# Performance work log

Measured on AMD Instinct MI355X. Metric: run time of the kernel, lower is better.

Reference implementation:

```python
import jax, jax.numpy as jnp
import numpy as np

EMBED_DIM = 1024
NUM_HEADS = 16
DEPTH = 12
HEAD_DIM = EMBED_DIM // NUM_HEADS // 2  # 32
LAMBDA_INIT = float(0.8 - 0.6 * np.exp(-0.3 * DEPTH))
B, T = 2, 2048


def setup_inputs() -> dict:
    key = jax.random.key(0)
    ks = jax.random.split(key, 10)
    s = 0.02
    return {
        "query": jax.random.normal(ks[0], (B, T, EMBED_DIM), jnp.float32),
        "Wq": jax.random.normal(ks[1], (EMBED_DIM, EMBED_DIM), jnp.float32) * s,
        "Wk": jax.random.normal(ks[2], (EMBED_DIM, EMBED_DIM), jnp.float32) * s,
        "Wv": jax.random.normal(ks[3], (EMBED_DIM, EMBED_DIM), jnp.float32) * s,
        "Wo": jax.random.normal(ks[4], (EMBED_DIM, EMBED_DIM), jnp.float32) * s,
        "lambda_q1": jax.random.normal(ks[5], (HEAD_DIM,), jnp.float32) * 0.1,
        "lambda_k1": jax.random.normal(ks[6], (HEAD_DIM,), jnp.float32) * 0.1,
        "lambda_q2": jax.random.normal(ks[7], (HEAD_DIM,), jnp.float32) * 0.1,
        "lambda_k2": jax.random.normal(ks[8], (HEAD_DIM,), jnp.float32) * 0.1,
        "subln_w": jnp.ones((2 * HEAD_DIM,), jnp.float32),
    }


def reference(query, Wq, Wk, Wv, Wo, lambda_q1, lambda_k1, lambda_q2, lambda_k2, subln_w):
    Bsz, Tt, E = query.shape
    H, hd = NUM_HEADS, HEAD_DIM
    scaling = hd ** -0.5
    # projections (torch Linear: x @ W.T), W stored [out, in]
    q = jnp.einsum('bte,fe->btf', query, Wq).reshape(Bsz, Tt, 2 * H, hd).transpose(0, 2, 1, 3)
    k = jnp.einsum('bse,fe->bsf', query, Wk).reshape(Bsz, Tt, 2 * H, hd).transpose(0, 2, 1, 3)
    v = jnp.einsum('bse,fe->bsf', query, Wv).reshape(Bsz, Tt, H, 2 * hd).transpose(0, 2, 1, 3)
    q = q * scaling
    # dual attention map [B, 2H, T, T], softmax in fp32
    scores = jnp.einsum('bhtd,bhsd->bhts', q, k)
    attn_w = jax.nn.softmax(scores.astype(jnp.float32), axis=-1).astype(q.dtype)
    # learned lambda
    lam1 = jnp.exp(jnp.sum(lambda_q1 * lambda_k1))
    lam2 = jnp.exp(jnp.sum(lambda_q2 * lambda_k2))
    lam = lam1 - lam2 + LAMBDA_INIT
    aw = attn_w.reshape(Bsz, H, 2, Tt, Tt)
    aw = aw[:, :, 0] - lam * aw[:, :, 1]  # [B, H, T, T]
    attn = jnp.einsum('bhts,bhsd->bhtd', aw, v)  # [B, H, T, 2*hd]
    # RMSNorm over last dim (fp32), eps=1e-5, elementwise affine
    x32 = attn.astype(jnp.float32)
    normed = (x32 * jax.lax.rsqrt(jnp.mean(x32 * x32, axis=-1, keepdims=True) + 1e-5)).astype(attn.dtype)
    attn = normed * subln_w
    attn = attn * (1.0 - LAMBDA_INIT)
    out = attn.transpose(0, 2, 1, 3).reshape(Bsz, Tt, H * 2 * hd)
    return jnp.einsum('bte,fe->btf', out, Wo)
```

## Files before the change

### kernel.cpp

```cpp
#include <hip/hip_runtime.h>

typedef short bf16x8 __attribute__((ext_vector_type(8)));
typedef float f32x4 __attribute__((ext_vector_type(4)));
typedef float f32x16 __attribute__((ext_vector_type(16)));
typedef unsigned short ushort_t;
typedef unsigned int uint32;

#define LAMBDA_INIT 0.7836057665316245f
#define TT 2048
#define EE 1024

__device__ __forceinline__ ushort_t f2bf(float x) {
  uint32 b = __float_as_uint(x);
  b += 0x7fffu + ((b >> 16) & 1u);
  return (ushort_t)(b >> 16);
}

__device__ __forceinline__ uint32 cvtpk(float lo, float hi) {
  uint32 r;
  asm("v_cvt_pk_bf16_f32 %0, %1, %2" : "=v"(r) : "v"(lo), "v"(hi));
  return r;
}

__device__ __forceinline__ float fexp2(float x) {
#if __has_builtin(__builtin_amdgcn_exp2f)
  return __builtin_amdgcn_exp2f(x);
#else
  return exp2f(x);
#endif
}

__device__ __forceinline__ bf16x8 mkfrag(uint32 a, uint32 b, uint32 c, uint32 d) {
  union { uint32 w[4]; bf16x8 v; } u;
  u.w[0] = a; u.w[1] = b; u.w[2] = c; u.w[3] = d;
  return u.v;
}

__device__ __forceinline__ void gload16(const void* g, void* l) {
  __builtin_amdgcn_global_load_lds(
      (const __attribute__((address_space(1))) uint32*)g,
      (__attribute__((address_space(3))) uint32*)l, 16, 0, 0);
}

__global__ __launch_bounds__(256) void cvt_all(const float* __restrict__ X,
                                               const float* __restrict__ Wq,
                                               const float* __restrict__ Wk,
                                               const float* __restrict__ Wv,
                                               const float* __restrict__ Wo,
                                               ushort_t* __restrict__ out) {
  const int i = blockIdx.x * 256 + threadIdx.x;
  const float* src;
  int off;
  if (i < 1048576)      { src = X;  off = 0; }
  else if (i < 1310720) { src = Wq; off = 1048576; }
  else if (i < 1572864) { src = Wk; off = 1310720; }
  else if (i < 1835008) { src = Wv; off = 1572864; }
  else                  { src = Wo; off = 1835008; }
  const float4 v = reinterpret_cast<const float4*>(src)[i - off];
  ushort4 o;
  o.x = f2bf(v.x); o.y = f2bf(v.y); o.z = f2bf(v.z); o.w = f2bf(v.w);
  reinterpret_cast<ushort4*>(out)[i] = o;
}

template <int MODE>
__global__ __launch_bounds__(256) void gemm_bt(const ushort_t* __restrict__ A,
                                               const ushort_t* __restrict__ B,
                                               void* __restrict__ C,
                                               int M, int N, int K, float scale) {
  __shared__ ushort_t As[128 * 32];
  __shared__ ushort_t Bs[128 * 32];
  const int tid = threadIdx.x;
  const int lane = tid & 63, wid = tid >> 6;
  const int wr = wid >> 1, wc = wid & 1;
  const int r16 = lane & 15, g = lane >> 4;
  const int m0 = blockIdx.x * 128, n0 = blockIdx.y * 128;
  f32x4 acc[4][4] = {};
  for (int k0 = 0; k0 < K; k0 += 32) {
#pragma unroll
    for (int c = 0; c < 2; ++c) {
      int eo = wid * 1024 + c * 512 + lane * 8;
      int row = eo >> 5, col = eo & 31;
      gload16(A + (size_t)(m0 + row) * K + k0 + col, As + wid * 1024 + c * 512);
      gload16(B + (size_t)(n0 + row) * K + k0 + col, Bs + wid * 1024 + c * 512);
    }
    __syncthreads();
    bf16x8 af[4], bfg[4];
#pragma unroll
    for (int m = 0; m < 4; ++m)
      af[m] = *reinterpret_cast<const bf16x8*>(As + (wr * 64 + m * 16 + r16) * 32 + g * 8);
#pragma unroll
    for (int n = 0; n < 4; ++n)
      bfg[n] = *reinterpret_cast<const bf16x8*>(Bs + (wc * 64 + n * 16 + r16) * 32 + g * 8);
#pragma unroll
    for (int m = 0; m < 4; ++m)
#pragma unroll
      for (int n = 0; n < 4; ++n)
        acc[m][n] = __builtin_amdgcn_mfma_f32_16x16x32_bf16(af[m], bfg[n], acc[m][n], 0, 0, 0);
    __syncthreads();
  }
#pragma unroll
  for (int m = 0; m < 4; ++m)
#pragma unroll
    for (int n = 0; n < 4; ++n) {
      if constexpr (MODE == 3) {
        const size_t MN = (size_t)4096 * EE;
        const int col = n0 + wc * 64 + n * 16 + r16;
        const int seg = col >> 10;
        const int cl = col & 1023;
        if (seg == 2) {
          int row0 = m0 + wr * 64 + m * 16 + g * 4;
          int bb = row0 >> 11, t0v = row0 & (TT - 1);
          ushort4 pk;
          pk.x = f2bf(acc[m][n][0]); pk.y = f2bf(acc[m][n][1]);
          pk.z = f2bf(acc[m][n][2]); pk.w = f2bf(acc[m][n][3]);
          *reinterpret_cast<ushort4*>(
              (ushort_t*)C + 2 * MN +
              ((size_t)(bb * 16 + (cl >> 6)) * 64 + (cl & 63)) * TT + t0v) = pk;
        } else {
          const float sc = (seg == 0) ? scale : 1.0f;
          const size_t base = (size_t)seg * MN;
#pragma unroll
          for (int r = 0; r < 4; ++r) {
            int row = m0 + wr * 64 + m * 16 + g * 4 + r;
            ((ushort_t*)C)[base + (size_t)row * EE + cl] = f2bf(acc[m][n][r] * sc);
          }
        }
      } else {
#pragma unroll
        for (int r = 0; r < 4; ++r) {
          int row = m0 + wr * 64 + m * 16 + g * 4 + r;
          int col = n0 + wc * 64 + n * 16 + r16;
          reinterpret_cast<float*>(C)[(size_t)row * N + col] = acc[m][n][r] * scale;
        }
      }
    }
}


#define PHALF(sv, lacc, oT0, oT1, vf)                                                   \
  do {                                                                                  \
    float p_[16];                                                                       \
    _Pragma("unroll") for (int i_ = 0; i_ < 16; ++i_) p_[i_] = fexp2(sv[i_]);           \
    lacc += (((p_[0] + p_[1]) + (p_[2] + p_[3])) + ((p_[4] + p_[5]) + (p_[6] + p_[7]))) \
          + (((p_[8] + p_[9]) + (p_[10] + p_[11])) +                                    \
             ((p_[12] + p_[13]) + (p_[14] + p_[15])));                                  \
    auto wA_ = __builtin_amdgcn_permlane32_swap((int)cvtpk(p_[0], p_[1]),               \
                                                (int)cvtpk(p_[4], p_[5]), false, false);\
    auto wB_ = __builtin_amdgcn_permlane32_swap((int)cvtpk(p_[2], p_[3]),               \
                                                (int)cvtpk(p_[6], p_[7]), false, false);\
    auto wC_ = __builtin_amdgcn_permlane32_swap((int)cvtpk(p_[8], p_[9]),               \
                                                (int)cvtpk(p_[12], p_[13]), false, false);\
    auto wD_ = __builtin_amdgcn_permlane32_swap((int)cvtpk(p_[10], p_[11]),             \
                                                (int)cvtpk(p_[14], p_[15]), false, false);\
    bf16x8 pa0_ = mkfrag(wA_[0], wB_[0], wA_[1], wB_[1]);                               \
    bf16x8 pa1_ = mkfrag(wC_[0], wD_[0], wC_[1], wD_[1]);                               \
    oT0 = __builtin_amdgcn_mfma_f32_32x32x16_bf16(pa0_, vf[0][0], oT0, 0, 0, 0);        \
    oT0 = __builtin_amdgcn_mfma_f32_32x32x16_bf16(pa1_, vf[1][0], oT0, 0, 0, 0);        \
    oT1 = __builtin_amdgcn_mfma_f32_32x32x16_bf16(pa0_, vf[0][1], oT1, 0, 0, 0);        \
    oT1 = __builtin_amdgcn_mfma_f32_32x32x16_bf16(pa1_, vf[1][1], oT1, 0, 0, 0);        \
  } while (0)

#define STAGE(bi, kv0)                                                                  \
  do {                                                                                  \
    const int r8_ = lane >> 3;                                                          \
    const int g_ = (lane & 7) ^ r8_;                                                    \
    _Pragma("unroll") for (int c2_ = 0; c2_ < 2; ++c2_) {                               \
      const int c_ = wid * 2 + c2_;                                                     \
      gload16(Kg + (size_t)((kv0) + c_ * 8 + r8_) * EE + g_ * 8,                        \
              Ksm[bi] + c_ * 512);                                                      \
      gload16(Vg + (size_t)(c_ * 8 + r8_) * TT + (kv0) + g_ * 8,                        \
              Vsm[bi] + c_ * 512);                                                      \
    }                                                                                   \
  } while (0)

__global__ __launch_bounds__(256, 2) void attn_fused(
    const ushort_t* __restrict__ Q, const ushort_t* __restrict__ K,
    const ushort_t* __restrict__ Vt,
    const float* __restrict__ lq1, const float* __restrict__ lk1,
    const float* __restrict__ lq2, const float* __restrict__ lk2,
    const float* __restrict__ w, ushort_t* __restrict__ X2) {
  __shared__ ushort_t Ksm[2][64 * 64];
  __shared__ ushort_t Vsm[2][64 * 64];
  const int tid = threadIdx.x, lane = tid & 63, wid = tid >> 6;
  const int l31 = lane & 31, hh = lane >> 5;
  const int bid = blockIdx.x;
  const int slice = (bid & 7) + 8 * (bid >> 7);
  const int qb = (bid >> 3) & 15;
  const int bb = slice >> 4, h = slice & 15;
  const int q0 = qb * 128 + wid * 32;

  float prod = (lane < 32) ? lq1[l31] * lk1[l31] : lq2[l31] * lk2[l31];
#pragma unroll
  for (int off = 1; off < 32; off <<= 1) prod += __shfl_xor(prod, off, 32);
  const float lam = __expf(__shfl(prod, 0, 64)) - __expf(__shfl(prod, 32, 64)) + LAMBDA_INIT;

  const ushort_t* Qp = Q + (size_t)(bb * TT + q0 + l31) * EE + h * 64 + hh * 8;
  const bf16x8 qf00 = *reinterpret_cast<const bf16x8*>(Qp);
  const bf16x8 qf01 = *reinterpret_cast<const bf16x8*>(Qp + 16);
  const bf16x8 qf10 = *reinterpret_cast<const bf16x8*>(Qp + 32);
  const bf16x8 qf11 = *reinterpret_cast<const bf16x8*>(Qp + 48);

  const ushort_t* Kg = K + (size_t)bb * TT * EE + h * 64;
  const ushort_t* Vg = Vt + (size_t)(bb * 16 + h) * 64 * TT;
  const int swz = (l31 & 7) << 3;

  f32x16 o00 = {}, o01 = {}, o10 = {}, o11 = {};
  float l0 = 0.f, l1 = 0.f;

  STAGE(0, 0);
  for (int it = 0; it < TT / 64; ++it) {
    const int cur = it & 1;
    __syncthreads();
    if (it + 1 < TT / 64) STAGE(cur ^ 1, (it + 1) * 64);

    const ushort_t* Kt_ = Ksm[cur];
    const ushort_t* Vt_ = Vsm[cur];
#pragma unroll
    for (int s = 0; s < 2; ++s) {
      bf16x8 kf[2][2], vf[2][2];
#pragma unroll
      for (int hf = 0; hf < 2; ++hf)
#pragma unroll
        for (int ks = 0; ks < 2; ++ks)
          kf[hf][ks] = *reinterpret_cast<const bf16x8*>(
              Kt_ + (s * 32 + l31) * 64 + ((hf * 32 + ks * 16 + hh * 8) ^ swz));
#pragma unroll
      for (int ks = 0; ks < 2; ++ks)
#pragma unroll
        for (int dc = 0; dc < 2; ++dc)
          vf[ks][dc] = *reinterpret_cast<const bf16x8*>(
              Vt_ + (dc * 32 + l31) * 64 + ((s * 32 + ks * 16 + hh * 8) ^ swz));

      __builtin_amdgcn_s_setprio(1);
      const f32x16 zz = {};
      f32x16 s0_ = __builtin_amdgcn_mfma_f32_32x32x16_bf16(kf[0][0], qf00, zz, 0, 0, 0);
      s0_ = __builtin_amdgcn_mfma_f32_32x32x16_bf16(kf[0][1], qf01, s0_, 0, 0, 0);
      f32x16 s1_ = __builtin_amdgcn_mfma_f32_32x32x16_bf16(kf[1][0], qf10, zz, 0, 0, 0);
      s1_ = __builtin_amdgcn_mfma_f32_32x32x16_bf16(kf[1][1], qf11, s1_, 0, 0, 0);
      __builtin_amdgcn_s_setprio(0);
      PHALF(s0_, l0, o00, o01, vf);
      PHALF(s1_, l1, o10, o11, vf);
    }
  }

  {
    auto t0 = __builtin_amdgcn_permlane32_swap(__float_as_int(l0), __float_as_int(l0),
                                               false, false);
    l0 = __int_as_float(t0[0]) + __int_as_float(t0[1]);
    auto t1 = __builtin_amdgcn_permlane32_swap(__float_as_int(l1), __float_as_int(l1),
                                               false, false);
    l1 = __int_as_float(t1[0]) + __int_as_float(t1[1]);
  }

  const float w0v = w[l31];
  const float w1v = w[32 + l31];
#pragma unroll
  for (int r = 0; r < 16; ++r) {
    const int qrel = (r & 3) + 8 * (r >> 2) + 4 * hh;
    const float il0 = 1.0f / __shfl(l0, qrel, 64);
    const float il1 = lam / __shfl(l1, qrel, 64);
    const float x0 = o00[r] * il0 - o10[r] * il1;
    const float x1 = o01[r] * il0 - o11[r] * il1;
    float ss = x0 * x0 + x1 * x1;
#pragma unroll
    for (int off = 1; off < 32; off <<= 1) ss += __shfl_xor(ss, off, 64);
    const float sc = rsqrtf(ss * (1.0f / 64.0f) + 1e-5f) * (1.0f - LAMBDA_INIT);
    const size_t ob = (size_t)(bb * TT + q0 + qrel) * EE + h * 64 + l31;
    X2[ob] = f2bf(x0 * sc * w0v);
    X2[ob + 32] = f2bf(x1 * sc * w1v);
  }
}

extern "C" void kernel_launch(void* const* d_in, const int* in_sizes, int n_in,
                              void* d_out, int out_size, void* d_ws, size_t ws_size,
                              hipStream_t stream) {
  const float* X = (const float*)d_in[0];
  const float* Wq = (const float*)d_in[1];
  const float* Wk = (const float*)d_in[2];
  const float* Wv = (const float*)d_in[3];
  const float* Wo = (const float*)d_in[4];
  const float* lq1 = (const float*)d_in[5];
  const float* lk1 = (const float*)d_in[6];
  const float* lq2 = (const float*)d_in[7];
  const float* lk2 = (const float*)d_in[8];
  const float* slw = (const float*)d_in[9];

  const int M = 4096, E = EE;

  ushort_t* Xb = (ushort_t*)d_ws;
  ushort_t* Wqb = Xb + (size_t)M * E;
  ushort_t* Wob = Wqb + (size_t)3 * E * E;
  ushort_t* Qb = Wob + (size_t)E * E;
  ushort_t* Kb = Qb + (size_t)M * E;
  ushort_t* Vtb = Kb + (size_t)M * E;
  ushort_t* X2 = Vtb + (size_t)M * E;

  cvt_all<<<8192, 256, 0, stream>>>(X, Wq, Wk, Wv, Wo, Xb);

  gemm_bt<3><<<dim3(M / 128, 3072 / 128), 256, 0, stream>>>(
      Xb, Wqb, Qb, M, 3072, E, 0.17677669529663687f * 1.4426950408889634f);

  attn_fused<<<512, 256, 0, stream>>>(Qb, Kb, Vtb, lq1, lk1, lq2, lk2, slw, X2);

  gemm_bt<0><<<dim3(M / 128, E / 128), 256, 0, stream>>>(X2, Wob, d_out, M, E, E, 1.0f);
}
```

Measured before the change: 140.8 us.

## Replace QKV projection GEMM with 256x256 double-buffered swizzled-LDS kernel

Adds a dedicated QKV projection kernel that uses 256x256 output tiles with 512 threads, BK=64 and double-buffered LDS. The LDS layout is XOR-swizzled to avoid bank conflicts, global loads for the next tile are interleaved with MFMA chunks under s_setprio, and the grid is remapped so neighbouring blocks share tiles. The goal is more data reuse per block and hiding of load latency in the largest GEMM. The cost is a large register footprint (an 8x4 accumulator per wave) and only 192 blocks, which may leave some of the 256 CUs idle. The generic gemm_bt loses its MODE template and is kept only for the output projection.

```diff
diff --git a/kernel.cpp b/kernel.cpp
--- a/kernel.cpp
+++ b/kernel.cpp
@@ -62,10 +62,9 @@
   reinterpret_cast<ushort4*>(out)[i] = o;
 }
 
-template <int MODE>
 __global__ __launch_bounds__(256) void gemm_bt(const ushort_t* __restrict__ A,
                                                const ushort_t* __restrict__ B,
-                                               void* __restrict__ C,
+                                               float* __restrict__ C,
                                                int M, int N, int K, float scale) {
   __shared__ ushort_t As[128 * 32];
   __shared__ ushort_t Bs[128 * 32];
@@ -101,41 +100,130 @@
 #pragma unroll
   for (int m = 0; m < 4; ++m)
 #pragma unroll
+    for (int n = 0; n < 4; ++n)
+#pragma unroll
+      for (int r = 0; r < 4; ++r) {
+        int row = m0 + wr * 64 + m * 16 + g * 4 + r;
+        int col = n0 + wc * 64 + n * 16 + r16;
+        C[(size_t)row * N + col] = acc[m][n][r] * scale;
+      }
+}
+
+#define SHALF(Sbase, Gbase)                                                  \
+  do {                                                                       \
+    _Pragma("unroll") for (int j_ = 0; j_ < 2; ++j_) {                       \
+      const int c_ = wid * 2 + j_;                                           \
+      gload16((Gbase) + (size_t)(c_ * 8 + (lane >> 3)) * EE +                \
+                  (((lane & 7) ^ (lane >> 3)) << 3),                         \
+              (Sbase) + c_ * 512);                                           \
+    }                                                                        \
+  } while (0)
+
+#define CHUNK(mp)                                                            \
+  do {                                                                       \
+    __builtin_amdgcn_s_setprio(1);                                           \
+    _Pragma("unroll") for (int mm_ = 0; mm_ < 2; ++mm_) {                    \
+      const int m_ = (mp) * 2 + mm_;                                         \
+      _Pragma("unroll") for (int n_ = 0; n_ < 4; ++n_) {                     \
+        acc[m_][n_] = __builtin_amdgcn_mfma_f32_16x16x32_bf16(               \
+            af[m_][0], bfr[n_][0], acc[m_][n_], 0, 0, 0);                    \
+        acc[m_][n_] = __builtin_amdgcn_mfma_f32_16x16x32_bf16(               \
+            af[m_][1], bfr[n_][1], acc[m_][n_], 0, 0, 0);                    \
+      }                                                                      \
+    }                                                                        \
+    __builtin_amdgcn_s_setprio(0);                                           \
+  } while (0)
+
+__global__ __launch_bounds__(512, 2) void qkv_gemm256(const ushort_t* __restrict__ A,
+                                                      const ushort_t* __restrict__ B,
+                                                      ushort_t* __restrict__ C,
+                                                      float scale) {
+  __shared__ ushort_t Asm[2][16384];
+  __shared__ ushort_t Bsm[2][16384];
+  const int NKT = EE / 64;
+  const int tid = threadIdx.x, lane = tid & 63, wid = tid >> 6;
+  const int wr = wid >> 2, wc = wid & 3;
+  const int r16 = lane & 15, g = lane >> 4;
+  const int w = (blockIdx.x & 7) * 24 + (blockIdx.x >> 3);
+  const int bx = w & 15, by = w >> 4;
+  const int m0 = bx * 256, n0 = by * 256;
+  const ushort_t* Ab = A + (size_t)m0 * EE;
+  const ushort_t* Bb = B + (size_t)n0 * EE;
+
+#pragma unroll
+  for (int kt = 0; kt < 2; ++kt) {
+    SHALF(Asm[kt], Ab + kt * 64);
+    SHALF(Asm[kt] + 8192, Ab + (size_t)128 * EE + kt * 64);
+    SHALF(Bsm[kt], Bb + kt * 64);
+    SHALF(Bsm[kt] + 8192, Bb + (size_t)128 * EE + kt * 64);
+  }
+
+  f32x4 acc[8][4] = {};
+  for (int t = 0; t < NKT; ++t) {
+    const int b = t & 1;
+    if (t < NKT - 1) asm volatile("s_waitcnt vmcnt(8)" ::: "memory");
+    else             asm volatile("s_waitcnt vmcnt(0)" ::: "memory");
+    __builtin_amdgcn_s_barrier();
+    asm volatile("" ::: "memory");
+    bf16x8 af[8][2], bfr[4][2];
+#pragma unroll
+    for (int m = 0; m < 8; ++m) {
+      const int row = wr * 128 + m * 16 + r16;
+#pragma unroll
+      for (int kk = 0; kk < 2; ++kk)
+        af[m][kk] = *reinterpret_cast<const bf16x8*>(
+            Asm[b] + row * 64 + (((kk * 4 + g) ^ (r16 & 7)) << 3));
+    }
+#pragma unroll
     for (int n = 0; n < 4; ++n) {
-      if constexpr (MODE == 3) {
-        const size_t MN = (size_t)4096 * EE;
-        const int col = n0 + wc * 64 + n * 16 + r16;
-        const int seg = col >> 10;
-        const int cl = col & 1023;
-        if (seg == 2) {
-          int row0 = m0 + wr * 64 + m * 16 + g * 4;
-          int bb = row0 >> 11, t0v = row0 & (TT - 1);
-          ushort4 pk;
-          pk.x = f2bf(acc[m][n][0]); pk.y = f2bf(acc[m][n][1]);
-          pk.z = f2bf(acc[m][n][2]); pk.w = f2bf(acc[m][n][3]);
-          *reinterpret_cast<ushort4*>(
-              (ushort_t*)C + 2 * MN +
-              ((size_t)(bb * 16 + (cl >> 6)) * 64 + (cl & 63)) * TT + t0v) = pk;
-        } else {
-          const float sc = (seg == 0) ? scale : 1.0f;
-          const size_t base = (size_t)seg * MN;
-#pragma unroll
-          for (int r = 0; r < 4; ++r) {
-            int row = m0 + wr * 64 + m * 16 + g * 4 + r;
-            ((ushort_t*)C)[base + (size_t)row * EE + cl] = f2bf(acc[m][n][r] * sc);
-          }
-        }
+      const int row = wc * 64 + n * 16 + r16;
+#pragma unroll
+      for (int kk = 0; kk < 2; ++kk)
+        bfr[n][kk] = *reinterpret_cast<const bf16x8*>(
+            Bsm[b] + row * 64 + (((kk * 4 + g) ^ (r16 & 7)) << 3));
+    }
+    asm volatile("s_waitcnt lgkmcnt(0)" ::: "memory");
+    __builtin_amdgcn_s_barrier();
+    asm volatile("" ::: "memory");
+    const int ts = t + 2;
+    const bool st = ts < NKT;
+    if (st) SHALF(Asm[b], Ab + ts * 64);
+    CHUNK(0);
+    if (st) SHALF(Asm[b] + 8192, Ab + (size_t)128 * EE + ts * 64);
+    CHUNK(1);
+    if (st) SHALF(Bsm[b], Bb + ts * 64);
+    CHUNK(2);
+    if (st) SHALF(Bsm[b] + 8192, Bb + (size_t)128 * EE + ts * 64);
+    CHUNK(3);
+  }
+
+  const size_t MN = (size_t)4096 * EE;
+#pragma unroll
+  for (int m = 0; m < 8; ++m)
+#pragma unroll
+    for (int n = 0; n < 4; ++n) {
+      const int col = n0 + wc * 64 + n * 16 + r16;
+      const int seg = col >> 10;
+      const int cl = col & 1023;
+      if (seg == 2) {
+        int row0 = m0 + wr * 128 + m * 16 + g * 4;
+        int bb2 = row0 >> 11, t0v = row0 & (TT - 1);
+        ushort4 pk;
+        pk.x = f2bf(acc[m][n][0]); pk.y = f2bf(acc[m][n][1]);
+        pk.z = f2bf(acc[m][n][2]); pk.w = f2bf(acc[m][n][3]);
+        *reinterpret_cast<ushort4*>(
+            C + 2 * MN + ((size_t)(bb2 * 16 + (cl >> 6)) * 64 + (cl & 63)) * TT + t0v) = pk;
       } else {
+        const float sc = (seg == 0) ? scale : 1.0f;
+        const size_t base = (size_t)seg * MN;
 #pragma unroll
         for (int r = 0; r < 4; ++r) {
-          int row = m0 + wr * 64 + m * 16 + g * 4 + r;
-          int col = n0 + wc * 64 + n * 16 + r16;
-          reinterpret_cast<float*>(C)[(size_t)row * N + col] = acc[m][n][r] * scale;
+          int row = m0 + wr * 128 + m * 16 + g * 4 + r;
+          C[base + (size_t)row * EE + cl] = f2bf(acc[m][n][r] * sc);
         }
       }
     }
 }
-
 
 #define PHALF(sv, lacc, oT0, oT1, vf)                                                   \
   do {                                                                                  \
@@ -297,10 +385,11 @@
 
   cvt_all<<<8192, 256, 0, stream>>>(X, Wq, Wk, Wv, Wo, Xb);
 
-  gemm_bt<3><<<dim3(M / 128, 3072 / 128), 256, 0, stream>>>(
-      Xb, Wqb, Qb, M, 3072, E, 0.17677669529663687f * 1.4426950408889634f);
+  qkv_gemm256<<<192, 512, 0, stream>>>(Xb, Wqb, Qb,
+                                       0.17677669529663687f * 1.4426950408889634f);
 
   attn_fused<<<512, 256, 0, stream>>>(Qb, Kb, Vtb, lq1, lk1, lq2, lk2, slw, X2);
 
-  gemm_bt<0><<<dim3(M / 128, E / 128), 256, 0, stream>>>(X2, Wob, d_out, M, E, E, 1.0f);
-}
+  gemm_bt<<<dim3(M / 128, E / 128), 256, 0, stream>>>(X2, Wob, (float*)d_out, M, E, E,
+                                                      1.0f);
+}
```

Result: faster. 137.3 us (-2.5%).
